# Performance work log

Hardware: AMD Instinct MI355X
Metric: run time of the kernel (lower is better)

The kernel has to match this reference:

```python
import jax, jax.numpy as jnp
import numpy as np

WINDOW_SIZE = 2
SOFTMAX_TEMP = 0.01
WIDTH = 320
EPS = 1e-12  # F.normalize default eps


def _l2norm(x, axis):
    n = jnp.sqrt(jnp.sum(x * x, axis=axis, keepdims=True))
    return x / jnp.maximum(n, EPS)


def setup_inputs() -> dict:
    key = jax.random.key(0)
    k1, k2, k3, k4 = jax.random.split(key, 4)
    BW, C, N, S = 4, 256, 1024, 1
    return {
        "keypoint_scores": jax.random.uniform(k1, (BW, S, N), dtype=jnp.float32),
        "keypoint_desc": jax.random.normal(k2, (BW, C, N), dtype=jnp.float32),
        "desc_dense": jax.random.normal(k3, (BW, C, WIDTH, WIDTH), dtype=jnp.float32),
        "keypoint_coords": jax.random.uniform(k4, (BW, N, 2), dtype=jnp.float32),
    }


def reference(keypoint_scores, keypoint_desc, desc_dense, keypoint_coords):
    BW, C, N = keypoint_desc.shape
    B = BW // WINDOW_SIZE
    P = B * (WINDOW_SIZE - 1)  # number of (src, tgt) pairs

    # dense source pixel coordinates (u=col, v=row), matching torch meshgrid 'ij'
    idx = jnp.arange(WIDTH * WIDTH)
    coords = jnp.stack([(idx % WIDTH).astype(jnp.float32),
                        (idx // WIDTH).astype(jnp.float32)], axis=1)  # (HW, 2)

    # pair indexing: for window i, targets are i*w+1 .. i*w+w-1, source is i*w
    tgt_ids = jnp.array([i * WINDOW_SIZE + j for i in range(B)
                         for j in range(1, WINDOW_SIZE)], dtype=jnp.int32)
    src_ids = (tgt_ids // WINDOW_SIZE) * WINDOW_SIZE

    # normalized dense source descriptors: (B, C, HW)
    src_dense = desc_dense[::WINDOW_SIZE].reshape(B, C, -1)
    src_un = _l2norm(src_dense, axis=1)
    src_sel = src_un[tgt_ids // WINDOW_SIZE]  # (P, C, HW)

    # normalized target keypoint descriptors: (P, C, N)
    tgt_n = _l2norm(keypoint_desc[tgt_ids], axis=1)

    # QK^T over descriptor channel: (P, N, HW)
    match_vals = jnp.einsum('pcn,pcm->pnm', tgt_n, src_sel)
    soft = jax.nn.softmax(match_vals / SOFTMAX_TEMP, axis=2)

    # soft-argmax coordinates: (P, N, 2)
    pseudo_coords = jnp.einsum('pnm,md->pnd', soft, coords)

    match_weights = keypoint_scores[tgt_ids]  # (P, S, N)
    return pseudo_coords, match_weights, tgt_ids, src_ids
```

## Files before the change

kernel.cpp:

```cpp
#include <hip/hip_runtime.h>
#include <stdint.h>

#define HW_      102400
#define C_       256
#define N_       1024
#define P_       2
#define CHUNKS_  64
#define CHUNK_PX 1600
#define ITERS_   25
#define NB_      4
#define K2_      144.269504088896340f
#define MOFF_    (-72.134752044448170f)

typedef __attribute__((ext_vector_type(8))) short bf16x8;
typedef __attribute__((ext_vector_type(4))) float f32x4;

#define WS_TGT_OFF  0
#define WS_PAR_OFF  1048576

__device__ __forceinline__ uint32_t packbf(float a, float b) {
  uint32_t r;
  asm("v_cvt_pk_bf16_f32 %0, %1, %2" : "=v"(r) : "v"(a), "v"(b));
  return r;
}
__device__ __forceinline__ float fexp2(float x) {
  return __builtin_amdgcn_exp2f(x);
}

__global__ __launch_bounds__(256)
void k_pre(const float* __restrict__ kdesc, const float* __restrict__ kscores,
           uint16_t* __restrict__ tgt, float* __restrict__ out) {
  const int t = blockIdx.x * 256 + threadIdx.x;
  const int p = t >> 10, n = t & 1023;
  const float* src = kdesc + (size_t)(p * 2 + 1) * C_ * N_ + n;
  float s = 0.f;
  #pragma unroll 16
  for (int c = 0; c < C_; ++c) { const float v = src[c * N_]; s = fmaf(v, v, s); }
  const float inv = 1.f / fmaxf(sqrtf(s), 1e-12f);
  uint32_t* dst = (uint32_t*)(tgt + (size_t)t * C_);
  #pragma unroll 4
  for (int c8 = 0; c8 < C_; c8 += 8) {
    uint4 wv;
    wv.x = packbf(src[(c8 + 0) * N_] * inv, src[(c8 + 1) * N_] * inv);
    wv.y = packbf(src[(c8 + 2) * N_] * inv, src[(c8 + 3) * N_] * inv);
    wv.z = packbf(src[(c8 + 4) * N_] * inv, src[(c8 + 5) * N_] * inv);
    wv.w = packbf(src[(c8 + 6) * N_] * inv, src[(c8 + 7) * N_] * inv);
    *(uint4*)&dst[c8 / 2] = wv;
  }
  out[4096 + t] = kscores[(p * 2 + 1) * N_ + n];
}

__global__ __launch_bounds__(512, 2)
void k_main(const float* __restrict__ dense, const uint16_t* __restrict__ tgt,
            float4* __restrict__ partials) {
  __shared__ uint32_t lds[2 * 64 * 128];
  __shared__ float4 part4[8][16];
  __shared__ float4 invt4[2][16];

  const int bid   = blockIdx.x;
  const int xcd   = bid & 7;
  const int rr    = bid >> 3;
  const int grp   = xcd + 8 * (rr >> 2);
  const int nb    = rr & 3;
  const int p     = grp >> 6;
  const int chunk = grp & 63;

  const int t    = threadIdx.x;
  const int lane = t & 63;
  const int w    = t >> 6;
  const int l15  = lane & 15;
  const int g4   = lane >> 4;
  const int h    = w & 1;
  const int q    = w >> 1;

  const float* plane = dense + (size_t)(p * 2) * C_ * HW_;

  bf16x8 Bf[4][8];
  const int nbase = nb * 256 + q * 64;
  #pragma unroll
  for (int j = 0; j < 4; ++j) {
    const uint16_t* tp = tgt + (size_t)(p * N_ + nbase + j * 16 + l15) * C_ + g4 * 8;
    #pragma unroll
    for (int k = 0; k < 8; ++k) Bf[j][k] = *(const bf16x8*)(tp + k * 32);
  }

  float stS[4], stU[4], stV[4];
  #pragma unroll
  for (int j = 0; j < 4; ++j) { stS[j] = 0.f; stU[j] = 0.f; stV[j] = 0.f; }

  const int mi   = (t & 15) * 4;
  const int c8   = (t >> 4) * 8;
  const int wcol = (t >> 4) * 4;
  const int px0  = chunk * CHUNK_PX;

  const int row0 = h * 32 + l15;
  const int swr  = (row0 & 7) << 2;
  const int lr0  = h * 32 + g4 * 4;

  uint32_t* bufR = lds;
  uint32_t* bufW = lds + 64 * 128;

  float fva[8][4];

  {
    const int px = px0 + mi;
    #pragma unroll
    for (int j = 0; j < 8; ++j) {
      float4 v = *(const float4*)(plane + (size_t)(c8 + j) * HW_ + px);
      fva[j][0] = v.x; fva[j][1] = v.y; fva[j][2] = v.z; fva[j][3] = v.w;
    }
    float ps[4];
    #pragma unroll
    for (int i = 0; i < 4; ++i) {
      const int row = mi + i;
      uint4 wv;
      wv.x = packbf(fva[0][i], fva[1][i]);
      wv.y = packbf(fva[2][i], fva[3][i]);
      wv.z = packbf(fva[4][i], fva[5][i]);
      wv.w = packbf(fva[6][i], fva[7][i]);
      *(uint4*)&bufR[row * 128 + (wcol ^ ((row & 7) << 2))] = wv;
      float s = 0.f;
      #pragma unroll
      for (int j = 0; j < 8; ++j) s = fmaf(fva[j][i], fva[j][i], s);
      ps[i] = s;
    }
    #pragma unroll
    for (int i = 0; i < 4; ++i) {
      ps[i] += __shfl_xor(ps[i], 16, 64);
      ps[i] += __shfl_xor(ps[i], 32, 64);
    }
    if (g4 == 0) part4[w][l15] = make_float4(ps[0], ps[1], ps[2], ps[3]);
  }
  __syncthreads();
  if (w == 0) {
    float s = 0.f;
    #pragma unroll
    for (int j = 0; j < 8; ++j) s += ((const float*)part4)[j * 64 + lane];
    ((float*)invt4)[lane] = 1.f / fmaxf(sqrtf(s), 1e-12f);
  }
  __syncthreads();

  for (int iter = 0; iter < ITERS_; ++iter) {
    const bool more = (iter + 1 < ITERS_);

    if (more) {
      const int px = px0 + (iter + 1) * 64 + mi;
      #pragma unroll
      for (int j = 0; j < 8; ++j) {
        float4 v = *(const float4*)(plane + (size_t)(c8 + j) * HW_ + px);
        fva[j][0] = v.x; fva[j][1] = v.y; fva[j][2] = v.z; fva[j][3] = v.w;
      }
    }

    f32x4 acc[4][2];
    #pragma unroll
    for (int j = 0; j < 4; ++j) {
      acc[j][0] = (f32x4){0.f, 0.f, 0.f, 0.f};
      acc[j][1] = (f32x4){0.f, 0.f, 0.f, 0.f};
    }
    #pragma unroll
    for (int k = 0; k < 8; ++k) {
      const int col = (k * 16 + g4 * 4) ^ swr;
      bf16x8 a0 = *(const bf16x8*)&bufR[row0 * 128 + col];
      bf16x8 a1 = *(const bf16x8*)&bufR[(row0 + 16) * 128 + col];
      #pragma unroll
      for (int j = 0; j < 4; ++j) {
        acc[j][0] = __builtin_amdgcn_mfma_f32_16x16x32_bf16(a0, Bf[j][k], acc[j][0], 0, 0, 0);
        acc[j][1] = __builtin_amdgcn_mfma_f32_16x16x32_bf16(a1, Bf[j][k], acc[j][1], 0, 0, 0);
      }
    }

    const int slot = iter & 1;
    float kv[8];
    {
      float4 iv0 = invt4[slot][lr0 >> 2];
      float4 iv1 = invt4[slot][(lr0 >> 2) + 4];
      kv[0] = K2_ * iv0.x; kv[1] = K2_ * iv0.y; kv[2] = K2_ * iv0.z; kv[3] = K2_ * iv0.w;
      kv[4] = K2_ * iv1.x; kv[5] = K2_ * iv1.y; kv[6] = K2_ * iv1.z; kv[7] = K2_ * iv1.w;
    }
    const int rb = iter * 64 + lr0;
    #pragma unroll
    for (int s = 0; s < 2; ++s) {
      #pragma unroll
      for (int e = 0; e < 4; ++e) {
        const int r  = rb + s * 16 + e;
        const int vl = (r * 6554) >> 21;
        const float vf = (float)(chunk * 5 + vl);
        const float uf = (float)(r - vl * 320);
        const float kve = kv[s * 4 + e];
        #pragma unroll
        for (int j = 0; j < 4; ++j) {
          const float ev = fexp2(fmaf(kve, acc[j][s][e], MOFF_));
          stS[j] += ev;
          stU[j] = fmaf(ev, uf, stU[j]);
          stV[j] = fmaf(ev, vf, stV[j]);
        }
      }
    }

    if (more) {
      float ps[4];
      #pragma unroll
      for (int i = 0; i < 4; ++i) {
        const int row = mi + i;
        uint4 wv;
        wv.x = packbf(fva[0][i], fva[1][i]);
        wv.y = packbf(fva[2][i], fva[3][i]);
        wv.z = packbf(fva[4][i], fva[5][i]);
        wv.w = packbf(fva[6][i], fva[7][i]);
        *(uint4*)&bufW[row * 128 + (wcol ^ ((row & 7) << 2))] = wv;
        float s = 0.f;
        #pragma unroll
        for (int j = 0; j < 8; ++j) s = fmaf(fva[j][i], fva[j][i], s);
        ps[i] = s;
      }
      #pragma unroll
      for (int i = 0; i < 4; ++i) {
        ps[i] += __shfl_xor(ps[i], 16, 64);
        ps[i] += __shfl_xor(ps[i], 32, 64);
      }
      if (g4 == 0) part4[w][l15] = make_float4(ps[0], ps[1], ps[2], ps[3]);
    }
    __syncthreads();
    if (more && w == 0) {
      float s = 0.f;
      #pragma unroll
      for (int j = 0; j < 8; ++j) s += ((const float*)part4)[j * 64 + lane];
      ((float*)invt4)[((iter + 1) & 1) * 64 + lane] = 1.f / fmaxf(sqrtf(s), 1e-12f);
    }
    __syncthreads();
    uint32_t* tmp = bufR; bufR = bufW; bufW = tmp;
  }

  #pragma unroll
  for (int j = 0; j < 4; ++j) {
    float S = stS[j], U = stU[j], V = stV[j];
    S += __shfl_xor(S, 16, 64); U += __shfl_xor(U, 16, 64); V += __shfl_xor(V, 16, 64);
    S += __shfl_xor(S, 32, 64); U += __shfl_xor(U, 32, 64); V += __shfl_xor(V, 32, 64);
    if (lane < 16) {
      const int n = nbase + j * 16 + l15;
      partials[((size_t)(p * CHUNKS_ + chunk) * 2 + h) * N_ + n] = make_float4(S, U, V, 0.f);
    }
  }
}

__global__ void k_final(const float4* __restrict__ partials, float* __restrict__ out) {
  const int t = blockIdx.x * blockDim.x + threadIdx.x;
  const int p = t >> 10, n = t & 1023;
  float S = 0.f, U = 0.f, V = 0.f;
  #pragma unroll 4
  for (int s = 0; s < 2 * CHUNKS_; ++s) {
    const float4 v = partials[((size_t)p * 2 * CHUNKS_ + s) * N_ + n];
    S += v.x; U += v.y; V += v.z;
  }
  out[(size_t)(p * N_ + n) * 2 + 0] = U / S;
  out[(size_t)(p * N_ + n) * 2 + 1] = V / S;
  if (t < 4) {
    const float ids[4] = {1.f, 3.f, 0.f, 2.f};
    out[6144 + t] = ids[t];
  }
}

extern "C" void kernel_launch(void* const* d_in, const int* in_sizes, int n_in,
                              void* d_out, int out_size, void* d_ws, size_t ws_size,
                              hipStream_t stream) {
  const float* kscores = (const float*)d_in[0];
  const float* kdesc   = (const float*)d_in[1];
  const float* dense   = (const float*)d_in[2];
  float* out = (float*)d_out;

  char* ws = (char*)d_ws;
  uint16_t* tgt = (uint16_t*)(ws + WS_TGT_OFF);
  float4*   par = (float4*)(ws + WS_PAR_OFF);

  k_pre<<<(P_ * N_) / 256, 256, 0, stream>>>(kdesc, kscores, tgt, out);
  k_main<<<P_ * NB_ * CHUNKS_, 512, 0, stream>>>(dense, tgt, par);
  k_final<<<(P_ * N_) / 256, 256, 0, stream>>>(par, out);
}
```

Baseline: 222.6 us.

## Compute pixel norms from bf16 LDS fragments in-wave, dropping extra barrier

Per-pixel L2 norms are now computed inside each wave from the bf16 A-fragments it already reads for the MFMA, reduced with lane shuffles, instead of from fp32 values through a shared-memory partial-sum stage with a second __syncthreads per iteration. The LDS swizzle also changes to XOR in higher row bits. This removes one block barrier and the serial wave-0 reduction per tile, but adds VALU unpack and FMA work in the MFMA loop. Norms now come from bf16-rounded values, which changes numerics slightly.

```diff
diff --git a/kernel.cpp b/kernel.cpp
--- a/kernel.cpp
+++ b/kernel.cpp
@@ -14,6 +14,7 @@
 
 typedef __attribute__((ext_vector_type(8))) short bf16x8;
 typedef __attribute__((ext_vector_type(4))) float f32x4;
+typedef __attribute__((ext_vector_type(4))) uint32_t u32x4;
 
 #define WS_TGT_OFF  0
 #define WS_PAR_OFF  1048576
@@ -54,8 +55,6 @@
 void k_main(const float* __restrict__ dense, const uint16_t* __restrict__ tgt,
             float4* __restrict__ partials) {
   __shared__ uint32_t lds[2 * 64 * 128];
-  __shared__ float4 part4[8][16];
-  __shared__ float4 invt4[2][16];
 
   const int bid   = blockIdx.x;
   const int xcd   = bid & 7;
@@ -93,9 +92,13 @@
   const int wcol = (t >> 4) * 4;
   const int px0  = chunk * CHUNK_PX;
 
-  const int row0 = h * 32 + l15;
-  const int swr  = (row0 & 7) << 2;
-  const int lr0  = h * 32 + g4 * 4;
+  const int row0  = h * 32 + l15;
+  const int row1  = row0 + 16;
+  const int sw0   = ((row0 ^ (row0 >> 3)) & 7) << 2;
+  const int sw1   = ((row1 ^ (row1 >> 3)) & 7) << 2;
+  const int base0 = row0 * 128;
+  const int base1 = row1 * 128;
+  const int lr0   = h * 32 + g4 * 4;
 
   uint32_t* bufR = lds;
   uint32_t* bufW = lds + 64 * 128;
@@ -109,34 +112,17 @@
       float4 v = *(const float4*)(plane + (size_t)(c8 + j) * HW_ + px);
       fva[j][0] = v.x; fva[j][1] = v.y; fva[j][2] = v.z; fva[j][3] = v.w;
     }
-    float ps[4];
     #pragma unroll
     for (int i = 0; i < 4; ++i) {
       const int row = mi + i;
+      const int sw  = ((row ^ (row >> 3)) & 7) << 2;
       uint4 wv;
       wv.x = packbf(fva[0][i], fva[1][i]);
       wv.y = packbf(fva[2][i], fva[3][i]);
       wv.z = packbf(fva[4][i], fva[5][i]);
       wv.w = packbf(fva[6][i], fva[7][i]);
-      *(uint4*)&bufR[row * 128 + (wcol ^ ((row & 7) << 2))] = wv;
-      float s = 0.f;
-      #pragma unroll
-      for (int j = 0; j < 8; ++j) s = fmaf(fva[j][i], fva[j][i], s);
-      ps[i] = s;
-    }
-    #pragma unroll
-    for (int i = 0; i < 4; ++i) {
-      ps[i] += __shfl_xor(ps[i], 16, 64);
-      ps[i] += __shfl_xor(ps[i], 32, 64);
-    }
-    if (g4 == 0) part4[w][l15] = make_float4(ps[0], ps[1], ps[2], ps[3]);
-  }
-  __syncthreads();
-  if (w == 0) {
-    float s = 0.f;
-    #pragma unroll
-    for (int j = 0; j < 8; ++j) s += ((const float*)part4)[j * 64 + lane];
-    ((float*)invt4)[lane] = 1.f / fmaxf(sqrtf(s), 1e-12f);
+      *(uint4*)&bufR[row * 128 + (wcol ^ sw)] = wv;
+    }
   }
   __syncthreads();
 
@@ -158,26 +144,42 @@
       acc[j][0] = (f32x4){0.f, 0.f, 0.f, 0.f};
       acc[j][1] = (f32x4){0.f, 0.f, 0.f, 0.f};
     }
+    float p0a = 0.f, p0b = 0.f, p1a = 0.f, p1b = 0.f;
     #pragma unroll
     for (int k = 0; k < 8; ++k) {
-      const int col = (k * 16 + g4 * 4) ^ swr;
-      bf16x8 a0 = *(const bf16x8*)&bufR[row0 * 128 + col];
-      bf16x8 a1 = *(const bf16x8*)&bufR[(row0 + 16) * 128 + col];
+      const int col = k * 16 + g4 * 4;
+      bf16x8 a0 = *(const bf16x8*)&bufR[base0 + (col ^ sw0)];
+      bf16x8 a1 = *(const bf16x8*)&bufR[base1 + (col ^ sw1)];
       #pragma unroll
       for (int j = 0; j < 4; ++j) {
         acc[j][0] = __builtin_amdgcn_mfma_f32_16x16x32_bf16(a0, Bf[j][k], acc[j][0], 0, 0, 0);
         acc[j][1] = __builtin_amdgcn_mfma_f32_16x16x32_bf16(a1, Bf[j][k], acc[j][1], 0, 0, 0);
       }
-    }
-
-    const int slot = iter & 1;
-    float kv[8];
-    {
-      float4 iv0 = invt4[slot][lr0 >> 2];
-      float4 iv1 = invt4[slot][(lr0 >> 2) + 4];
-      kv[0] = K2_ * iv0.x; kv[1] = K2_ * iv0.y; kv[2] = K2_ * iv0.z; kv[3] = K2_ * iv0.w;
-      kv[4] = K2_ * iv1.x; kv[5] = K2_ * iv1.y; kv[6] = K2_ * iv1.z; kv[7] = K2_ * iv1.w;
-    }
+      const u32x4 u0 = __builtin_bit_cast(u32x4, a0);
+      const u32x4 u1 = __builtin_bit_cast(u32x4, a1);
+      #pragma unroll
+      for (int d = 0; d < 4; ++d) {
+        const float l0 = __builtin_bit_cast(float, u0[d] << 16);
+        const float h0 = __builtin_bit_cast(float, u0[d] & 0xFFFF0000u);
+        const float l1 = __builtin_bit_cast(float, u1[d] << 16);
+        const float h1 = __builtin_bit_cast(float, u1[d] & 0xFFFF0000u);
+        p0a = fmaf(l0, l0, p0a); p0b = fmaf(h0, h0, p0b);
+        p1a = fmaf(l1, l1, p1a); p1b = fmaf(h1, h1, p1b);
+      }
+    }
+
+    float ps0 = p0a + p0b, ps1 = p1a + p1b;
+    ps0 += __shfl_xor(ps0, 16, 64); ps0 += __shfl_xor(ps0, 32, 64);
+    ps1 += __shfl_xor(ps1, 16, 64); ps1 += __shfl_xor(ps1, 32, 64);
+    const float inv0 = 1.f / fmaxf(sqrtf(ps0), 1e-12f);
+    const float inv1 = 1.f / fmaxf(sqrtf(ps1), 1e-12f);
+    float kv0[4], kv1[4];
+    #pragma unroll
+    for (int e = 0; e < 4; ++e) {
+      kv0[e] = K2_ * __shfl(inv0, g4 * 4 + e, 64);
+      kv1[e] = K2_ * __shfl(inv1, g4 * 4 + e, 64);
+    }
+
     const int rb = iter * 64 + lr0;
     #pragma unroll
     for (int s = 0; s < 2; ++s) {
@@ -187,7 +189,7 @@
         const int vl = (r * 6554) >> 21;
         const float vf = (float)(chunk * 5 + vl);
         const float uf = (float)(r - vl * 320);
-        const float kve = kv[s * 4 + e];
+        const float kve = s ? kv1[e] : kv0[e];
         #pragma unroll
         for (int j = 0; j < 4; ++j) {
           const float ev = fexp2(fmaf(kve, acc[j][s][e], MOFF_));
@@ -199,34 +201,17 @@
     }
 
     if (more) {
-      float ps[4];
       #pragma unroll
       for (int i = 0; i < 4; ++i) {
         const int row = mi + i;
+        const int sw  = ((row ^ (row >> 3)) & 7) << 2;
         uint4 wv;
         wv.x = packbf(fva[0][i], fva[1][i]);
         wv.y = packbf(fva[2][i], fva[3][i]);
         wv.z = packbf(fva[4][i], fva[5][i]);
         wv.w = packbf(fva[6][i], fva[7][i]);
-        *(uint4*)&bufW[row * 128 + (wcol ^ ((row & 7) << 2))] = wv;
-        float s = 0.f;
-        #pragma unroll
-        for (int j = 0; j < 8; ++j) s = fmaf(fva[j][i], fva[j][i], s);
-        ps[i] = s;
-      }
-      #pragma unroll
-      for (int i = 0; i < 4; ++i) {
-        ps[i] += __shfl_xor(ps[i], 16, 64);
-        ps[i] += __shfl_xor(ps[i], 32, 64);
-      }
-      if (g4 == 0) part4[w][l15] = make_float4(ps[0], ps[1], ps[2], ps[3]);
-    }
-    __syncthreads();
-    if (more && w == 0) {
-      float s = 0.f;
-      #pragma unroll
-      for (int j = 0; j < 8; ++j) s += ((const float*)part4)[j * 64 + lane];
-      ((float*)invt4)[((iter + 1) & 1) * 64 + lane] = 1.f / fmaxf(sqrtf(s), 1e-12f);
+        *(uint4*)&bufW[row * 128 + (wcol ^ sw)] = wv;
+      }
     }
     __syncthreads();
     uint32_t* tmp = bufR; bufR = bufW; bufW = tmp;
```

Measured after the change: 250.3 us. 12.4% more time.
